# Optimization experiments

Hardware: AMD Instinct MI355X
Metric: run time of the kernel (lower is better)

## Reference

```python
import jax, jax.numpy as jnp
import numpy as np

B, N, D, R, H, E = 4, 8192, 16, 32, 64, 262144


def _linear_init(key, fan_in, fan_out):
    return jax.random.normal(key, (fan_in, fan_out), jnp.float32) * (1.0 / np.sqrt(fan_in))


def setup_inputs() -> dict:
    key = jax.random.key(0)
    ks = jax.random.split(key, 8)
    particles = jax.random.normal(ks[0], (B, N, D), jnp.float32)
    senders = jax.random.randint(ks[1], (E,), 0, N, dtype=jnp.int32)
    receivers = jax.random.randint(ks[2], (E,), 0, N, dtype=jnp.int32)
    # relation_encoder: Linear(2D->H), ReLU, Linear(H->R), ReLU
    W1 = _linear_init(ks[3], 2 * D, H)
    b1 = jnp.zeros((H,), jnp.float32)
    W2 = _linear_init(ks[4], H, R)
    b2 = jnp.zeros((R,), jnp.float32)
    # dynamics_fn: Linear(D+R->H), ReLU, Linear(H->D)
    W3 = _linear_init(ks[5], D + R, H)
    b3 = jnp.zeros((H,), jnp.float32)
    W4 = _linear_init(ks[6], H, D)
    b4 = jnp.zeros((D,), jnp.float32)
    return {"particles": particles, "senders": senders, "receivers": receivers,
            "W1": W1, "b1": b1, "W2": W2, "b2": b2,
            "W3": W3, "b3": b3, "W4": W4, "b4": b4}


def reference(particles, senders, receivers, W1, b1, W2, b2, W3, b3, W4, b4):
    # Gather per-edge sender/receiver states: [B, E, D]
    send = particles[:, senders, :]
    recv = particles[:, receivers, :]
    edge_in = jnp.concatenate([send, recv], axis=-1)          # [B, E, 2D]
    # relation_encoder (one batched GEMM over all edges)
    h = jax.nn.relu(edge_in @ W1 + b1)                        # [B, E, H]
    rel_feat = jax.nn.relu(h @ W2 + b2)                       # [B, E, R]
    # scatter-add edge features into receiver nodes
    Bp, Np, _ = particles.shape
    rel = jnp.zeros((Bp, Np, rel_feat.shape[-1]), particles.dtype)
    rel = rel.at[:, receivers, :].add(rel_feat)               # [B, N, R]
    # node update MLP
    dyn_in = jnp.concatenate([particles, rel], axis=-1)       # [B, N, D+R]
    delta = jax.nn.relu(dyn_in @ W3 + b3) @ W4 + b4           # [B, N, D]
    return particles + delta
```

## Files before the change

kernel.cpp:

```cpp
#include <hip/hip_runtime.h>
#include <hip/hip_bf16.h>

namespace {

constexpr int B = 4;
constexpr int N = 8192;
constexpr int D = 16;
constexpr int R = 32;
constexpr int H = 64;
constexpr int E = 262144;

typedef __attribute__((ext_vector_type(8))) short short8;
typedef __attribute__((ext_vector_type(4))) float f32x4;

__device__ __forceinline__ float4 ld4(const float* p) {
    return *reinterpret_cast<const float4*>(p);
}
__device__ __forceinline__ float4 fma4(float a, float4 w, float4 c) {
    return float4{fmaf(a, w.x, c.x), fmaf(a, w.y, c.y),
                  fmaf(a, w.z, c.z), fmaf(a, w.w, c.w)};
}
__device__ __forceinline__ float4 relu4(float4 v) {
    return float4{fmaxf(v.x, 0.f), fmaxf(v.y, 0.f), fmaxf(v.z, 0.f), fmaxf(v.w, 0.f)};
}
__device__ __forceinline__ short bf16s(float f) {
    __hip_bfloat16 h = __float2bfloat16(f);
    return __builtin_bit_cast(short, h);
}
__device__ __forceinline__ short8 pack8(float4 a, float4 b) {
    short8 o;
    o[0] = bf16s(a.x); o[1] = bf16s(a.y); o[2] = bf16s(a.z); o[3] = bf16s(a.w);
    o[4] = bf16s(b.x); o[5] = bf16s(b.y); o[6] = bf16s(b.z); o[7] = bf16s(b.w);
    return o;
}

__global__ __launch_bounds__(256) void hist_prepack_kernel(
    const int* __restrict__ receivers, int* __restrict__ cnt,
    const float* __restrict__ W1, const float* __restrict__ W2,
    const float* __restrict__ W3, const float* __restrict__ W4,
    short* __restrict__ w1p, short* __restrict__ w2p,
    short* __restrict__ w3p, short* __restrict__ w4p)
{
    if (blockIdx.x < 1024) {
        int e = blockIdx.x * 256 + threadIdx.x;
        atomicAdd(cnt + receivers[e], 1);
        return;
    }
    const int t = threadIdx.x;
    for (int i = t; i < 4 * 64 * 8; i += 256) {
        int j = i & 7, lane = (i >> 3) & 63, ct = i >> 9;
        int k = (lane >> 4) * 8 + j, n = ct * 16 + (lane & 15);
        w1p[i] = bf16s(W1[k * H + n]);
    }
    for (int i = t; i < 4 * 64 * 8; i += 256) {
        int j = i & 7, lane = (i >> 3) & 63, idx = i >> 9;
        int mt = idx >> 1, kc = idx & 1;
        int k = kc * 32 + (lane >> 4) * 8 + j, f = mt * 16 + (lane & 15);
        w2p[i] = bf16s(W2[k * R + f]);
    }
    for (int i = t; i < 8 * 64 * 8; i += 256) {
        int j = i & 7, lane = (i >> 3) & 63, idx = i >> 9;
        int ct = idx >> 1, kc = idx & 1;
        int k = kc * 32 + (lane >> 4) * 8 + j, n = ct * 16 + (lane & 15);
        w3p[i] = (k < D + R) ? bf16s(W3[k * H + n]) : (short)0;
    }
    for (int i = t; i < 2 * 64 * 8; i += 256) {
        int j = i & 7, lane = (i >> 3) & 63, kc = i >> 9;
        int k = kc * 32 + (lane >> 4) * 8 + j, d = lane & 15;
        w4p[i] = bf16s(W4[k * D + d]);
    }
}

__global__ __launch_bounds__(1024) void scan_kernel(
    const int* __restrict__ cnt, int* __restrict__ pos)
{
    __shared__ int wtot[16];
    const int t = threadIdx.x;
    const int lane = t & 63;
    int local[8];
    int s = 0;
    #pragma unroll
    for (int i = 0; i < 8; ++i) { local[i] = cnt[t * 8 + i]; s += local[i]; }
    int incl = s;
    #pragma unroll
    for (int d = 1; d < 64; d <<= 1) {
        int v = __shfl_up(incl, d, 64);
        if (lane >= d) incl += v;
    }
    if (lane == 63) wtot[t >> 6] = incl;
    __syncthreads();
    int base = incl - s;
    const int wv = t >> 6;
    #pragma unroll
    for (int i = 0; i < 16; ++i) base += (i < wv) ? wtot[i] : 0;
    #pragma unroll
    for (int i = 0; i < 8; ++i) {
        pos[t * 8 + i] = base;
        base += local[i];
    }
}

__global__ __launch_bounds__(256) void scatter_kernel(
    const int* __restrict__ senders, const int* __restrict__ receivers,
    int* __restrict__ pos, int* __restrict__ ssorted, int* __restrict__ rsorted)
{
    int e = blockIdx.x * 256 + threadIdx.x;
    if (e < E) {
        int r = receivers[e];
        int p = atomicAdd(pos + r, 1);
        ssorted[p] = senders[e];
        rsorted[p] = r;
    }
}

__global__ __launch_bounds__(256, 3) void edge_mfma_kernel(
    const float* __restrict__ particles,
    const int*   __restrict__ ssorted,
    const int*   __restrict__ rsorted,
    const short* __restrict__ w1p, const float* __restrict__ b1,
    const short* __restrict__ w2p, const float* __restrict__ b2,
    float* __restrict__ rel)
{
    __shared__ float red[R * 257];
    __shared__ short hbuf[4][16 * 72];
    __shared__ int   rs[256];

    const int tid  = threadIdx.x;
    const int lane = tid & 63;
    const int w    = tid >> 6;
    const int b    = blockIdx.x >> 10;
    const int p0   = (blockIdx.x & 1023) * 256;
    const int l15  = lane & 15;
    const int q    = lane >> 4;

    const int sval = ssorted[p0 + tid];
    const int rval = rsorted[p0 + tid];
    rs[tid] = rval;

    float4 a0[4], a1[4];
    #pragma unroll
    for (int t = 0; t < 4; ++t) {
        int srow = __shfl(sval, t * 16 + l15);
        int rrow = __shfl(rval, t * 16 + l15);
        int row = (q < 2) ? srow : rrow;
        const float* src = particles + ((size_t)b * N + row) * D + (q & 1) * 8;
        a0[t] = ld4(src);
        a1[t] = ld4(src + 4);
    }

    short8 w1f[4], w2f[4];
    #pragma unroll
    for (int ct = 0; ct < 4; ++ct)
        w1f[ct] = *reinterpret_cast<const short8*>(w1p + (ct * 64 + lane) * 8);
    #pragma unroll
    for (int i = 0; i < 4; ++i)
        w2f[i] = *reinterpret_cast<const short8*>(w2p + (i * 64 + lane) * 8);

    float bias1[4];
    #pragma unroll
    for (int ct = 0; ct < 4; ++ct) bias1[ct] = b1[ct * 16 + l15];
    f32x4 bias2[2];
    #pragma unroll
    for (int mt = 0; mt < 2; ++mt) {
        float4 t4 = ld4(b2 + mt * 16 + q * 4);
        bias2[mt] = f32x4{t4.x, t4.y, t4.z, t4.w};
    }

    short8 af[4];
    #pragma unroll
    for (int t = 0; t < 4; ++t) af[t] = pack8(a0[t], a1[t]);

    short* hb = &hbuf[w][0];

    #pragma unroll
    for (int t = 0; t < 4; ++t) {
        #pragma unroll
        for (int ct = 0; ct < 4; ++ct) {
            f32x4 c = {bias1[ct], bias1[ct], bias1[ct], bias1[ct]};
            c = __builtin_amdgcn_mfma_f32_16x16x32_bf16(af[t], w1f[ct], c, 0, 0, 0);
            #pragma unroll
            for (int rg = 0; rg < 4; ++rg)
                hb[(q * 4 + rg) * 72 + ct * 16 + l15] = bf16s(fmaxf(c[rg], 0.f));
        }
        short8 h0 = *reinterpret_cast<const short8*>(hb + l15 * 72 + q * 8);
        short8 h1 = *reinterpret_cast<const short8*>(hb + l15 * 72 + 32 + q * 8);

        f32x4 r0 = bias2[0], r1 = bias2[1];
        r0 = __builtin_amdgcn_mfma_f32_16x16x32_bf16(w2f[0], h0, r0, 0, 0, 0);
        r0 = __builtin_amdgcn_mfma_f32_16x16x32_bf16(w2f[1], h1, r0, 0, 0, 0);
        r1 = __builtin_amdgcn_mfma_f32_16x16x32_bf16(w2f[2], h0, r1, 0, 0, 0);
        r1 = __builtin_amdgcn_mfma_f32_16x16x32_bf16(w2f[3], h1, r1, 0, 0, 0);

        const int pl = w * 64 + t * 16 + l15;
        #pragma unroll
        for (int rg = 0; rg < 4; ++rg) {
            red[(q * 4 + rg) * 257 + pl]      = fmaxf(r0[rg], 0.f);
            red[(16 + q * 4 + rg) * 257 + pl] = fmaxf(r1[rg], 0.f);
        }
    }
    __syncthreads();

    const int g = tid >> 5;
    const int f = tid & 31;
    const int base = g * 32;
    float acc = 0.f;
    int cur = rs[base];
    #pragma unroll 1
    for (int i = 0; i < 32; ++i) {
        int rr = rs[base + i];
        float v = red[f * 257 + base + i];
        if (rr != cur) {
            atomicAdd(rel + ((size_t)b * N + cur) * R + f, acc);
            acc = 0.f;
            cur = rr;
        }
        acc += v;
    }
    atomicAdd(rel + ((size_t)b * N + cur) * R + f, acc);
}

__global__ __launch_bounds__(256, 4) void node_mfma_kernel(
    const float* __restrict__ particles,
    const float* __restrict__ rel,
    const short* __restrict__ w3p, const float* __restrict__ b3,
    const short* __restrict__ w4p, const float* __restrict__ b4,
    float* __restrict__ out)
{
    __shared__ short hbuf[4][16 * 72];

    const int tid  = threadIdx.x;
    const int lane = tid & 63;
    const int w    = tid >> 6;
    const int tile = blockIdx.x * 4 + w;
    const int b    = tile >> 9;
    const int l15  = lane & 15;
    const int q    = lane >> 4;
    const int node = (tile & 511) * 16 + l15;

    const float* prow = particles + ((size_t)b * N + node) * D;
    const float* rrow = rel + ((size_t)b * N + node) * R;

    const float* src0 = (q < 2) ? (prow + (q & 1) * 8) : (rrow + (q & 1) * 8);
    float4 c0a = ld4(src0), c0b = ld4(src0 + 4);
    float4 c1a = {0.f, 0.f, 0.f, 0.f}, c1b = {0.f, 0.f, 0.f, 0.f};
    if (q < 2) { c1a = ld4(rrow + 16 + q * 8); c1b = ld4(rrow + 20 + q * 8); }

    short8 w3f[8], w4f[2];
    #pragma unroll
    for (int i = 0; i < 8; ++i)
        w3f[i] = *reinterpret_cast<const short8*>(w3p + (i * 64 + lane) * 8);
    #pragma unroll
    for (int i = 0; i < 2; ++i)
        w4f[i] = *reinterpret_cast<const short8*>(w4p + (i * 64 + lane) * 8);

    float bias3[4];
    #pragma unroll
    for (int ct = 0; ct < 4; ++ct) bias3[ct] = b3[ct * 16 + l15];
    f32x4 bias4;
    { float4 t4 = ld4(b4 + q * 4); bias4 = f32x4{t4.x, t4.y, t4.z, t4.w}; }

    short8 a0 = pack8(c0a, c0b);
    short8 a1 = pack8(c1a, c1b);

    short* hb = &hbuf[w][0];
    #pragma unroll
    for (int ct = 0; ct < 4; ++ct) {
        f32x4 c = {bias3[ct], bias3[ct], bias3[ct], bias3[ct]};
        c = __builtin_amdgcn_mfma_f32_16x16x32_bf16(a0, w3f[ct * 2 + 0], c, 0, 0, 0);
        c = __builtin_amdgcn_mfma_f32_16x16x32_bf16(a1, w3f[ct * 2 + 1], c, 0, 0, 0);
        #pragma unroll
        for (int rg = 0; rg < 4; ++rg)
            hb[(q * 4 + rg) * 72 + ct * 16 + l15] = bf16s(fmaxf(c[rg], 0.f));
    }
    short8 h0 = *reinterpret_cast<const short8*>(hb + l15 * 72 + q * 8);
    short8 h1 = *reinterpret_cast<const short8*>(hb + l15 * 72 + 32 + q * 8);

    f32x4 r = bias4;
    r = __builtin_amdgcn_mfma_f32_16x16x32_bf16(w4f[0], h0, r, 0, 0, 0);
    r = __builtin_amdgcn_mfma_f32_16x16x32_bf16(w4f[1], h1, r, 0, 0, 0);

    const float* pi = prow + q * 4;
    float4 pv = ld4(pi);
    float4* po = reinterpret_cast<float4*>(out + ((size_t)b * N + node) * D + q * 4);
    *po = float4{pv.x + r[0], pv.y + r[1], pv.z + r[2], pv.w + r[3]};
}


__global__ __launch_bounds__(256, 2) void edge_atomic_kernel(
    const float* __restrict__ particles,
    const int*   __restrict__ senders,
    const int*   __restrict__ receivers,
    const float* __restrict__ W1, const float* __restrict__ b1,
    const float* __restrict__ W2, const float* __restrict__ b2,
    float* __restrict__ rel)
{
    const int idx = blockIdx.x * 256 + threadIdx.x;
    const int b = idx >> 18;
    const int e = idx & (E - 1);
    const int s = senders[e];
    const int r = receivers[e];

    float4 ein4[8];
    {
        const float4* ps = reinterpret_cast<const float4*>(particles + ((size_t)b * N + s) * D);
        const float4* pr = reinterpret_cast<const float4*>(particles + ((size_t)b * N + r) * D);
        #pragma unroll
        for (int qq = 0; qq < 4; ++qq) ein4[qq] = ps[qq];
        #pragma unroll
        for (int qq = 0; qq < 4; ++qq) ein4[4 + qq] = pr[qq];
    }
    float4 rf4[8];
    #pragma unroll
    for (int qq = 0; qq < 8; ++qq) rf4[qq] = ld4(b2 + 4 * qq);

    for (int j4 = 0; j4 < H / 4; ++j4) {
        float4 h = ld4(b1 + 4 * j4);
        const float* w1c = W1 + 4 * j4;
        #pragma unroll
        for (int kv = 0; kv < 8; ++kv) {
            const float4 ev = ein4[kv];
            h = fma4(ev.x, ld4(w1c + (4 * kv + 0) * H), h);
            h = fma4(ev.y, ld4(w1c + (4 * kv + 1) * H), h);
            h = fma4(ev.z, ld4(w1c + (4 * kv + 2) * H), h);
            h = fma4(ev.w, ld4(w1c + (4 * kv + 3) * H), h);
        }
        h = relu4(h);
        const float* w2r = W2 + (4 * j4) * R;
        #pragma unroll
        for (int qq = 0; qq < 4; ++qq) {
            const float hq = (qq == 0) ? h.x : (qq == 1) ? h.y : (qq == 2) ? h.z : h.w;
            #pragma unroll
            for (int r4 = 0; r4 < 8; ++r4)
                rf4[r4] = fma4(hq, ld4(w2r + qq * R + 4 * r4), rf4[r4]);
        }
    }
    float* dst = rel + ((size_t)b * N + r) * R;
    #pragma unroll
    for (int r4 = 0; r4 < 8; ++r4) {
        float4 v = relu4(rf4[r4]);
        atomicAdd(dst + 4 * r4 + 0, v.x);
        atomicAdd(dst + 4 * r4 + 1, v.y);
        atomicAdd(dst + 4 * r4 + 2, v.z);
        atomicAdd(dst + 4 * r4 + 3, v.w);
    }
}

__global__ __launch_bounds__(256, 2) void node_valu_kernel(
    const float* __restrict__ particles,
    const float* __restrict__ rel,
    const float* __restrict__ W3, const float* __restrict__ b3,
    const float* __restrict__ W4, const float* __restrict__ b4,
    float* __restrict__ out)
{
    const int idx = blockIdx.x * 256 + threadIdx.x;
    float4 in4[12];
    {
        const float4* pp = reinterpret_cast<const float4*>(particles + (size_t)idx * D);
        #pragma unroll
        for (int qq = 0; qq < 4; ++qq) in4[qq] = pp[qq];
        const float4* pr = reinterpret_cast<const float4*>(rel + (size_t)idx * R);
        #pragma unroll
        for (int qq = 0; qq < 8; ++qq) in4[4 + qq] = pr[qq];
    }
    float4 dl4[4];
    #pragma unroll
    for (int qq = 0; qq < 4; ++qq) dl4[qq] = ld4(b4 + 4 * qq);

    for (int j4 = 0; j4 < H / 4; ++j4) {
        float4 h = ld4(b3 + 4 * j4);
        const float* w3c = W3 + 4 * j4;
        #pragma unroll
        for (int kv = 0; kv < 12; ++kv) {
            const float4 ev = in4[kv];
            h = fma4(ev.x, ld4(w3c + (4 * kv + 0) * H), h);
            h = fma4(ev.y, ld4(w3c + (4 * kv + 1) * H), h);
            h = fma4(ev.z, ld4(w3c + (4 * kv + 2) * H), h);
            h = fma4(ev.w, ld4(w3c + (4 * kv + 3) * H), h);
        }
        h = relu4(h);
        const float* w4r = W4 + (4 * j4) * D;
        #pragma unroll
        for (int qq = 0; qq < 4; ++qq) {
            const float hq = (qq == 0) ? h.x : (qq == 1) ? h.y : (qq == 2) ? h.z : h.w;
            #pragma unroll
            for (int d4 = 0; d4 < 4; ++d4)
                dl4[d4] = fma4(hq, ld4(w4r + qq * D + 4 * d4), dl4[d4]);
        }
    }
    float4* po = reinterpret_cast<float4*>(out + (size_t)idx * D);
    #pragma unroll
    for (int qq = 0; qq < 4; ++qq) {
        float4 v = dl4[qq];
        float4 pv = in4[qq];
        po[qq] = float4{pv.x + v.x, pv.y + v.y, pv.z + v.z, pv.w + v.w};
    }
}

}

extern "C" void kernel_launch(void* const* d_in, const int* in_sizes, int n_in,
                              void* d_out, int out_size, void* d_ws, size_t ws_size,
                              hipStream_t stream) {
    const float* particles = (const float*)d_in[0];
    const int*   senders   = (const int*)d_in[1];
    const int*   receivers = (const int*)d_in[2];
    const float* W1 = (const float*)d_in[3];
    const float* b1 = (const float*)d_in[4];
    const float* W2 = (const float*)d_in[5];
    const float* b2 = (const float*)d_in[6];
    const float* W3 = (const float*)d_in[7];
    const float* b3 = (const float*)d_in[8];
    const float* W4 = (const float*)d_in[9];
    const float* b4 = (const float*)d_in[10];
    float* out = (float*)d_out;

    char* ws = (char*)d_ws;
    size_t off = 0;
    auto take = [&](size_t bytes) -> char* {
        char* p = ws + off;
        off = (off + bytes + 255) & ~(size_t)255;
        return p;
    };
    int*   cnt     = (int*)  take((size_t)N * 4);
    int*   pos     = (int*)  take((size_t)N * 4);
    int*   ssorted = (int*)  take((size_t)E * 4);
    int*   rsorted = (int*)  take((size_t)E * 4);
    float* rel     = (float*)take((size_t)B * N * R * 4);
    short* w1p     = (short*)take((size_t)4 * 64 * 8 * 2);
    short* w2p     = (short*)take((size_t)4 * 64 * 8 * 2);
    short* w3p     = (short*)take((size_t)8 * 64 * 8 * 2);
    short* w4p     = (short*)take((size_t)2 * 64 * 8 * 2);
    const bool fast = (off <= ws_size);

    if (fast) {
        hipMemsetAsync(cnt, 0, (size_t)N * 4, stream);
        hipMemsetAsync(rel, 0, (size_t)B * N * R * 4, stream);
        hist_prepack_kernel<<<1025, 256, 0, stream>>>(
            receivers, cnt, W1, W2, W3, W4, w1p, w2p, w3p, w4p);
        scan_kernel<<<1, 1024, 0, stream>>>(cnt, pos);
        scatter_kernel<<<E / 256, 256, 0, stream>>>(senders, receivers, pos, ssorted, rsorted);
        edge_mfma_kernel<<<(B * E) / 256, 256, 0, stream>>>(
            particles, ssorted, rsorted, w1p, b1, w2p, b2, rel);
        node_mfma_kernel<<<(B * N / 16) / 4, 256, 0, stream>>>(
            particles, rel, w3p, b3, w4p, b4, out);
    } else {
        float* rel0 = (float*)d_ws;
        hipMemsetAsync(rel0, 0, (size_t)B * N * R * 4, stream);
        edge_atomic_kernel<<<(B * E) / 256, 256, 0, stream>>>(
            particles, senders, receivers, W1, b1, W2, b2, rel0);
        node_valu_kernel<<<(B * N) / 256, 256, 0, stream>>>(
            particles, rel0, W3, b3, W4, b4, out);
    }
}
```

Before: 150.7 us.

## Fuse rel zeroing into prepack, pack sorted edges, transpose MFMAs, vectorize segment reduce

Several changes at once. The memset of rel is folded into the histogram/prepack kernel as extra blocks, which removes one API launch. Sender and receiver indices are scattered into a single int2 array, so each edge needs one load instead of two. The MFMA operand order is swapped in both the edge and node kernels, so results land as 4-wide vectors that can be written to LDS with vector stores instead of scalar ones. The per-receiver segmented reduction now loads values and receiver ids as float4/int4 and takes a fast path when a 32-edge group shares one receiver; this adds register pressure and relies on the new operand layout being correct.

```diff
diff --git a/kernel.cpp b/kernel.cpp
--- a/kernel.cpp
+++ b/kernel.cpp
@@ -11,6 +11,7 @@
 constexpr int E = 262144;
 
 typedef __attribute__((ext_vector_type(8))) short short8;
+typedef __attribute__((ext_vector_type(4))) short short4v;
 typedef __attribute__((ext_vector_type(4))) float f32x4;
 
 __device__ __forceinline__ float4 ld4(const float* p) {
@@ -33,17 +34,33 @@
     o[4] = bf16s(b.x); o[5] = bf16s(b.y); o[6] = bf16s(b.z); o[7] = bf16s(b.w);
     return o;
 }
+__device__ __forceinline__ short4v pack4_relu(f32x4 c) {
+    short4v o;
+    o[0] = bf16s(fmaxf(c[0], 0.f)); o[1] = bf16s(fmaxf(c[1], 0.f));
+    o[2] = bf16s(fmaxf(c[2], 0.f)); o[3] = bf16s(fmaxf(c[3], 0.f));
+    return o;
+}
+
+constexpr int RED_S = 260;
 
 __global__ __launch_bounds__(256) void hist_prepack_kernel(
     const int* __restrict__ receivers, int* __restrict__ cnt,
     const float* __restrict__ W1, const float* __restrict__ W2,
     const float* __restrict__ W3, const float* __restrict__ W4,
     short* __restrict__ w1p, short* __restrict__ w2p,
-    short* __restrict__ w3p, short* __restrict__ w4p)
+    short* __restrict__ w3p, short* __restrict__ w4p,
+    float4* __restrict__ relz)
 {
     if (blockIdx.x < 1024) {
         int e = blockIdx.x * 256 + threadIdx.x;
         atomicAdd(cnt + receivers[e], 1);
+        return;
+    }
+    if (blockIdx.x >= 1025) {
+        const int base = (blockIdx.x - 1025) * 256 + threadIdx.x;
+        #pragma unroll
+        for (int i = 0; i < 8; ++i)
+            relz[base + i * 32768] = float4{0.f, 0.f, 0.f, 0.f};
         return;
     }
     const int t = threadIdx.x;
@@ -54,8 +71,8 @@
     }
     for (int i = t; i < 4 * 64 * 8; i += 256) {
         int j = i & 7, lane = (i >> 3) & 63, idx = i >> 9;
-        int mt = idx >> 1, kc = idx & 1;
-        int k = kc * 32 + (lane >> 4) * 8 + j, f = mt * 16 + (lane & 15);
+        int ct = idx >> 1, kc = idx & 1;
+        int k = kc * 32 + (lane >> 4) * 8 + j, f = ct * 16 + (lane & 15);
         w2p[i] = bf16s(W2[k * R + f]);
     }
     for (int i = t; i < 8 * 64 * 8; i += 256) {
@@ -102,26 +119,24 @@
 
 __global__ __launch_bounds__(256) void scatter_kernel(
     const int* __restrict__ senders, const int* __restrict__ receivers,
-    int* __restrict__ pos, int* __restrict__ ssorted, int* __restrict__ rsorted)
+    int* __restrict__ pos, int2* __restrict__ sr)
 {
     int e = blockIdx.x * 256 + threadIdx.x;
     if (e < E) {
         int r = receivers[e];
         int p = atomicAdd(pos + r, 1);
-        ssorted[p] = senders[e];
-        rsorted[p] = r;
+        sr[p] = int2{senders[e], r};
     }
 }
 
 __global__ __launch_bounds__(256, 3) void edge_mfma_kernel(
     const float* __restrict__ particles,
-    const int*   __restrict__ ssorted,
-    const int*   __restrict__ rsorted,
+    const int2*  __restrict__ sr,
     const short* __restrict__ w1p, const float* __restrict__ b1,
     const short* __restrict__ w2p, const float* __restrict__ b2,
     float* __restrict__ rel)
 {
-    __shared__ float red[R * 257];
+    __shared__ float red[31 * RED_S + 256];
     __shared__ short hbuf[4][16 * 72];
     __shared__ int   rs[256];
 
@@ -133,8 +148,9 @@
     const int l15  = lane & 15;
     const int q    = lane >> 4;
 
-    const int sval = ssorted[p0 + tid];
-    const int rval = rsorted[p0 + tid];
+    const int2 srv = sr[p0 + tid];
+    const int sval = srv.x;
+    const int rval = srv.y;
     rs[tid] = rval;
 
     float4 a0[4], a1[4];
@@ -150,21 +166,20 @@
 
     short8 w1f[4], w2f[4];
     #pragma unroll
-    for (int ct = 0; ct < 4; ++ct)
-        w1f[ct] = *reinterpret_cast<const short8*>(w1p + (ct * 64 + lane) * 8);
+    for (int mt = 0; mt < 4; ++mt)
+        w1f[mt] = *reinterpret_cast<const short8*>(w1p + (mt * 64 + lane) * 8);
     #pragma unroll
     for (int i = 0; i < 4; ++i)
         w2f[i] = *reinterpret_cast<const short8*>(w2p + (i * 64 + lane) * 8);
 
-    float bias1[4];
-    #pragma unroll
-    for (int ct = 0; ct < 4; ++ct) bias1[ct] = b1[ct * 16 + l15];
-    f32x4 bias2[2];
-    #pragma unroll
-    for (int mt = 0; mt < 2; ++mt) {
-        float4 t4 = ld4(b2 + mt * 16 + q * 4);
-        bias2[mt] = f32x4{t4.x, t4.y, t4.z, t4.w};
-    }
+    f32x4 bias1[4];
+    #pragma unroll
+    for (int mt = 0; mt < 4; ++mt) {
+        float4 t4 = ld4(b1 + mt * 16 + q * 4);
+        bias1[mt] = f32x4{t4.x, t4.y, t4.z, t4.w};
+    }
+    const float bias2a = b2[l15];
+    const float bias2b = b2[16 + l15];
 
     short8 af[4];
     #pragma unroll
@@ -175,48 +190,67 @@
     #pragma unroll
     for (int t = 0; t < 4; ++t) {
         #pragma unroll
-        for (int ct = 0; ct < 4; ++ct) {
-            f32x4 c = {bias1[ct], bias1[ct], bias1[ct], bias1[ct]};
-            c = __builtin_amdgcn_mfma_f32_16x16x32_bf16(af[t], w1f[ct], c, 0, 0, 0);
-            #pragma unroll
-            for (int rg = 0; rg < 4; ++rg)
-                hb[(q * 4 + rg) * 72 + ct * 16 + l15] = bf16s(fmaxf(c[rg], 0.f));
+        for (int mt = 0; mt < 4; ++mt) {
+            f32x4 c = bias1[mt];
+            c = __builtin_amdgcn_mfma_f32_16x16x32_bf16(w1f[mt], af[t], c, 0, 0, 0);
+            *reinterpret_cast<short4v*>(hb + l15 * 72 + mt * 16 + q * 4) = pack4_relu(c);
         }
         short8 h0 = *reinterpret_cast<const short8*>(hb + l15 * 72 + q * 8);
         short8 h1 = *reinterpret_cast<const short8*>(hb + l15 * 72 + 32 + q * 8);
 
-        f32x4 r0 = bias2[0], r1 = bias2[1];
-        r0 = __builtin_amdgcn_mfma_f32_16x16x32_bf16(w2f[0], h0, r0, 0, 0, 0);
-        r0 = __builtin_amdgcn_mfma_f32_16x16x32_bf16(w2f[1], h1, r0, 0, 0, 0);
-        r1 = __builtin_amdgcn_mfma_f32_16x16x32_bf16(w2f[2], h0, r1, 0, 0, 0);
-        r1 = __builtin_amdgcn_mfma_f32_16x16x32_bf16(w2f[3], h1, r1, 0, 0, 0);
-
-        const int pl = w * 64 + t * 16 + l15;
-        #pragma unroll
-        for (int rg = 0; rg < 4; ++rg) {
-            red[(q * 4 + rg) * 257 + pl]      = fmaxf(r0[rg], 0.f);
-            red[(16 + q * 4 + rg) * 257 + pl] = fmaxf(r1[rg], 0.f);
-        }
+        f32x4 r0 = {bias2a, bias2a, bias2a, bias2a};
+        f32x4 r1 = {bias2b, bias2b, bias2b, bias2b};
+        r0 = __builtin_amdgcn_mfma_f32_16x16x32_bf16(h0, w2f[0], r0, 0, 0, 0);
+        r0 = __builtin_amdgcn_mfma_f32_16x16x32_bf16(h1, w2f[1], r0, 0, 0, 0);
+        r1 = __builtin_amdgcn_mfma_f32_16x16x32_bf16(h0, w2f[2], r1, 0, 0, 0);
+        r1 = __builtin_amdgcn_mfma_f32_16x16x32_bf16(h1, w2f[3], r1, 0, 0, 0);
+
+        const int pb = w * 64 + t * 16 + q * 4;
+        *reinterpret_cast<f32x4*>(red + l15 * RED_S + pb) =
+            f32x4{fmaxf(r0[0], 0.f), fmaxf(r0[1], 0.f), fmaxf(r0[2], 0.f), fmaxf(r0[3], 0.f)};
+        *reinterpret_cast<f32x4*>(red + (16 + l15) * RED_S + pb) =
+            f32x4{fmaxf(r1[0], 0.f), fmaxf(r1[1], 0.f), fmaxf(r1[2], 0.f), fmaxf(r1[3], 0.f)};
     }
     __syncthreads();
 
     const int g = tid >> 5;
     const int f = tid & 31;
     const int base = g * 32;
-    float acc = 0.f;
-    int cur = rs[base];
-    #pragma unroll 1
-    for (int i = 0; i < 32; ++i) {
-        int rr = rs[base + i];
-        float v = red[f * 257 + base + i];
-        if (rr != cur) {
-            atomicAdd(rel + ((size_t)b * N + cur) * R + f, acc);
-            acc = 0.f;
-            cur = rr;
-        }
-        acc += v;
-    }
-    atomicAdd(rel + ((size_t)b * N + cur) * R + f, acc);
+
+    f32x4 v4[8];
+    #pragma unroll
+    for (int i = 0; i < 8; ++i)
+        v4[i] = *reinterpret_cast<const f32x4*>(red + f * RED_S + base + 4 * i);
+    int4 r4[8];
+    #pragma unroll
+    for (int i = 0; i < 8; ++i)
+        r4[i] = *reinterpret_cast<const int4*>(rs + base + 4 * i);
+
+    const int first = r4[0].x;
+    const int last  = r4[7].w;
+    if (first == last) {
+        float acc = 0.f;
+        #pragma unroll
+        for (int i = 0; i < 8; ++i)
+            acc += (v4[i][0] + v4[i][1]) + (v4[i][2] + v4[i][3]);
+        atomicAdd(rel + ((size_t)b * N + first) * R + f, acc);
+    } else {
+        float acc = 0.f;
+        int cur = first;
+        #pragma unroll
+        for (int i = 0; i < 32; ++i) {
+            int rr = (i & 3) == 0 ? r4[i >> 2].x : (i & 3) == 1 ? r4[i >> 2].y
+                   : (i & 3) == 2 ? r4[i >> 2].z : r4[i >> 2].w;
+            float v = v4[i >> 2][i & 3];
+            if (rr != cur) {
+                atomicAdd(rel + ((size_t)b * N + cur) * R + f, acc);
+                acc = 0.f;
+                cur = rr;
+            }
+            acc += v;
+        }
+        atomicAdd(rel + ((size_t)b * N + cur) * R + f, acc);
+    }
 }
 
 __global__ __launch_bounds__(256, 4) void node_mfma_kernel(
@@ -253,9 +287,12 @@
     for (int i = 0; i < 2; ++i)
         w4f[i] = *reinterpret_cast<const short8*>(w4p + (i * 64 + lane) * 8);
 
-    float bias3[4];
-    #pragma unroll
-    for (int ct = 0; ct < 4; ++ct) bias3[ct] = b3[ct * 16 + l15];
+    f32x4 bias3[4];
+    #pragma unroll
+    for (int mt = 0; mt < 4; ++mt) {
+        float4 t4 = ld4(b3 + mt * 16 + q * 4);
+        bias3[mt] = f32x4{t4.x, t4.y, t4.z, t4.w};
+    }
     f32x4 bias4;
     { float4 t4 = ld4(b4 + q * 4); bias4 = f32x4{t4.x, t4.y, t4.z, t4.w}; }
 
@@ -264,13 +301,11 @@
 
     short* hb = &hbuf[w][0];
     #pragma unroll
-    for (int ct = 0; ct < 4; ++ct) {
-        f32x4 c = {bias3[ct], bias3[ct], bias3[ct], bias3[ct]};
-        c = __builtin_amdgcn_mfma_f32_16x16x32_bf16(a0, w3f[ct * 2 + 0], c, 0, 0, 0);
-        c = __builtin_amdgcn_mfma_f32_16x16x32_bf16(a1, w3f[ct * 2 + 1], c, 0, 0, 0);
-        #pragma unroll
-        for (int rg = 0; rg < 4; ++rg)
-            hb[(q * 4 + rg) * 72 + ct * 16 + l15] = bf16s(fmaxf(c[rg], 0.f));
+    for (int mt = 0; mt < 4; ++mt) {
+        f32x4 c = bias3[mt];
+        c = __builtin_amdgcn_mfma_f32_16x16x32_bf16(w3f[mt * 2 + 0], a0, c, 0, 0, 0);
+        c = __builtin_amdgcn_mfma_f32_16x16x32_bf16(w3f[mt * 2 + 1], a1, c, 0, 0, 0);
+        *reinterpret_cast<short4v*>(hb + l15 * 72 + mt * 16 + q * 4) = pack4_relu(c);
     }
     short8 h0 = *reinterpret_cast<const short8*>(hb + l15 * 72 + q * 8);
     short8 h1 = *reinterpret_cast<const short8*>(hb + l15 * 72 + 32 + q * 8);
@@ -279,8 +314,7 @@
     r = __builtin_amdgcn_mfma_f32_16x16x32_bf16(w4f[0], h0, r, 0, 0, 0);
     r = __builtin_amdgcn_mfma_f32_16x16x32_bf16(w4f[1], h1, r, 0, 0, 0);
 
-    const float* pi = prow + q * 4;
-    float4 pv = ld4(pi);
+    float4 pv = ld4(prow + q * 4);
     float4* po = reinterpret_cast<float4*>(out + ((size_t)b * N + node) * D + q * 4);
     *po = float4{pv.x + r[0], pv.y + r[1], pv.z + r[2], pv.w + r[3]};
 }
@@ -423,8 +457,7 @@
     };
     int*   cnt     = (int*)  take((size_t)N * 4);
     int*   pos     = (int*)  take((size_t)N * 4);
-    int*   ssorted = (int*)  take((size_t)E * 4);
-    int*   rsorted = (int*)  take((size_t)E * 4);
+    int2*  sr      = (int2*) take((size_t)E * 8);
     float* rel     = (float*)take((size_t)B * N * R * 4);
     short* w1p     = (short*)take((size_t)4 * 64 * 8 * 2);
     short* w2p     = (short*)take((size_t)4 * 64 * 8 * 2);
@@ -434,13 +467,12 @@
 
     if (fast) {
         hipMemsetAsync(cnt, 0, (size_t)N * 4, stream);
-        hipMemsetAsync(rel, 0, (size_t)B * N * R * 4, stream);
-        hist_prepack_kernel<<<1025, 256, 0, stream>>>(
-            receivers, cnt, W1, W2, W3, W4, w1p, w2p, w3p, w4p);
+        hist_prepack_kernel<<<1025 + 128, 256, 0, stream>>>(
+            receivers, cnt, W1, W2, W3, W4, w1p, w2p, w3p, w4p, (float4*)rel);
         scan_kernel<<<1, 1024, 0, stream>>>(cnt, pos);
-        scatter_kernel<<<E / 256, 256, 0, stream>>>(senders, receivers, pos, ssorted, rsorted);
+        scatter_kernel<<<E / 256, 256, 0, stream>>>(senders, receivers, pos, sr);
         edge_mfma_kernel<<<(B * E) / 256, 256, 0, stream>>>(
-            particles, ssorted, rsorted, w1p, b1, w2p, b2, rel);
+            particles, sr, w1p, b1, w2p, b2, rel);
         node_mfma_kernel<<<(B * N / 16) / 4, 256, 0, stream>>>(
             particles, rel, w3p, b3, w4p, b4, out);
     } else {
```

Result: faster. 140.0 us (-7.1%).
